# Performance work log

Measured on AMD Instinct MI355X. Metric: run time of the kernel, lower is better.

## Reference

```python
import jax, jax.numpy as jnp
import numpy as np

B, T, I, H, O = 32, 2048, 512, 512, 256


def setup_inputs() -> dict:
    key = jax.random.key(0)
    ks = jax.random.split(key, 11)
    s_in = 1.0 / np.sqrt(I)  # torch Linear default init bound
    s_h = 1.0 / np.sqrt(H)

    def lin(k, shape, s):
        return jax.random.uniform(k, shape, jnp.float32, -s, s)

    return {
        "x": jax.random.normal(ks[0], (B, T, I), jnp.float32),
        "W_i": lin(ks[1], (H, I), s_in), "b_i": lin(ks[2], (H,), s_in),
        "W_f": lin(ks[3], (H, I), s_in), "b_f": lin(ks[4], (H,), s_in),
        "W_g": lin(ks[5], (H, I), s_in), "b_g": lin(ks[6], (H,), s_in),
        "W_o": lin(ks[7], (H, I), s_in), "b_o": lin(ks[8], (H,), s_in),
        "W_fc": lin(ks[9], (O, H), s_h), "b_fc": lin(ks[10], (O,), s_h),
    }


def reference(x, W_i, b_i, W_f, b_f, W_g, b_g, W_o, b_o, W_fc, b_fc):
    # NOTE: this module's gates depend on x only (not h), so all four gate
    # projections can be precomputed as one pass of GEMMs over [B,T,I].
    gi = jax.nn.sigmoid(jnp.einsum("bti,hi->bth", x, W_i) + b_i)
    gf = jax.nn.sigmoid(jnp.einsum("bti,hi->bth", x, W_f) + b_f)
    gg = jnp.tanh(jnp.einsum("bti,hi->bth", x, W_g) + b_g)
    go = jax.nn.sigmoid(jnp.einsum("bti,hi->bth", x, W_o) + b_o)

    # Sequential elementwise recurrence over time (time-major for scan).
    def step(carry, gates_t):
        _, c = carry
        i, f, g, o = gates_t
        c = f * c + i * g
        h = o * jnp.tanh(c)
        return (h, c), None

    init = (jnp.zeros((B, H), x.dtype), jnp.zeros((B, H), x.dtype))
    gates_tm = (gi.swapaxes(0, 1), gf.swapaxes(0, 1),
                gg.swapaxes(0, 1), go.swapaxes(0, 1))  # each [T,B,H]
    (h, _), _ = jax.lax.scan(step, init, gates_tm)

    return h @ W_fc.T + b_fc  # [B, O]
```

## Files before the change

kernel.cpp:

```cpp
#include <hip/hip_runtime.h>
#include <stdint.h>

#define DI 512
#define DH 512
#define DOUT 256
#define NB 32
#define NT 2048
#define MTOT (NB*NT)
#define NCHUNK 16
#define CLEN 128
#define BM 128
#define BN 64
#define BK 32

typedef unsigned short u16;
typedef __attribute__((ext_vector_type(8))) short bf16x8;
typedef __attribute__((ext_vector_type(4))) short s16x4;
typedef __attribute__((ext_vector_type(4))) float f32x4;

__device__ __forceinline__ u16 f2bf(float f) {
    union { float f; unsigned int u; } c; c.f = f;
    unsigned int u = c.u;
    u += 0x7fffu + ((u >> 16) & 1u);
    return (u16)(u >> 16);
}
__device__ __forceinline__ float bf2f(u16 h) {
    union { unsigned int u; float f; } c; c.u = ((unsigned int)h) << 16;
    return c.f;
}
__device__ __forceinline__ float sigm(float x) { return 1.0f / (1.0f + __expf(-x)); }
__device__ __forceinline__ float tanh_(float x) { return 1.0f - 2.0f / (__expf(2.0f * x) + 1.0f); }

__global__ void cvt_w3(const float* __restrict__ w0, const float* __restrict__ w1,
                       const float* __restrict__ w2, u16* __restrict__ out) {
    const int per = DH * DI / 4;
    int gid = blockIdx.x * blockDim.x + threadIdx.x;
    int wsel = gid / per;
    int i = gid - wsel * per;
    const float* src = (wsel == 0) ? w0 : (wsel == 1) ? w1 : w2;
    float4 v = reinterpret_cast<const float4*>(src)[i];
    ushort4 o;
    o.x = f2bf(v.x); o.y = f2bf(v.y); o.z = f2bf(v.z); o.w = f2bf(v.w);
    reinterpret_cast<ushort4*>(out + (size_t)wsel * DH * DI)[i] = o;
}

__global__ __launch_bounds__(256, 2)
void gate_gemm_scan(const float* __restrict__ X, const u16* __restrict__ W,
                    const float* __restrict__ b_i, const float* __restrict__ b_f,
                    const float* __restrict__ b_g,
                    float* __restrict__ Ach, float* __restrict__ Vch) {
    __shared__ __align__(16) union {
        struct { u16 sA[2][BM * BK]; u16 sB[2][3 * BN * BK]; } st;
        struct { u16 Ft[BN][132]; u16 Pt[BN][132]; float pa[256]; float pv[256]; } sc;
    } u;

    const int bid0 = blockIdx.x;
    const int swz = (bid0 & 7) * 512 + (bid0 >> 3);
    const int mtile = swz >> 3;
    const int ntile = swz & 7;
    const int m0 = mtile * BM;
    const int n0 = ntile * BN;

    const int tid = threadIdx.x;
    const int lane = tid & 63;
    const int ws = __builtin_amdgcn_readfirstlane(tid >> 6);
    const int wr = ws >> 1;
    const int wc = ws & 1;

    const int srow = lane >> 2;
    const int slot = lane & 3;
    const int fr = lane & 15;
    const int khalf = lane >> 4;

    const int rlA = ws * 32 + srow;
    const int swzslot = slot ^ ((rlA >> 1) & 3);
    const float* pXA = X + (size_t)(m0 + rlA) * DI + swzslot * 8;

    const int idx0 = ws * 3;
    const int g0 = idx0 >> 2, cc0 = idx0 & 3;
    const int rlB0 = cc0 * 16 + srow;
    const u16* gaB0 = W + (size_t)g0 * DH * DI + (size_t)(n0 + rlB0) * DI
                    + ((slot ^ ((rlB0 >> 1) & 3)) * 8);
    int dB[3];
    dB[0] = 0;
#pragma unroll
    for (int q = 1; q < 3; ++q) {
        const int idxq = idx0 + q;
        const int gq = idxq >> 2, ccq = idxq & 3;
        dB[q] = __builtin_amdgcn_readfirstlane((gq - g0) * (DH * DI) + (ccq - cc0) * 16 * DI);
    }

    const int rA = wr * 64 + fr;
    const int offA0 = rA * BK + ((khalf ^ ((rA >> 1) & 3)) * 8);
    const int rB = wc * 32 + fr;
    const int offB0 = rB * BK + ((khalf ^ ((rB >> 1) & 3)) * 8);

    float4 fa[2][2][2];

#define LOAD_A(P, KT) do {                                                          \
    _Pragma("unroll")                                                               \
    for (int s = 0; s < 2; ++s) {                                                   \
        fa[(P)][s][0] = *reinterpret_cast<const float4*>(pXA + (size_t)s * 16 * DI + (KT) * 32);     \
        fa[(P)][s][1] = *reinterpret_cast<const float4*>(pXA + (size_t)s * 16 * DI + (KT) * 32 + 4); \
    }                                                                               \
} while (0)

#define CVT_STAGE(P, CB) do {                                                       \
    _Pragma("unroll")                                                               \
    for (int s = 0; s < 2; ++s) {                                                   \
        unsigned int pk0, pk1, pk2, pk3;                                            \
        asm("v_cvt_pk_bf16_f32 %0, %1, %2" : "=v"(pk0) : "v"(fa[(P)][s][0].x), "v"(fa[(P)][s][0].y)); \
        asm("v_cvt_pk_bf16_f32 %0, %1, %2" : "=v"(pk1) : "v"(fa[(P)][s][0].z), "v"(fa[(P)][s][0].w)); \
        asm("v_cvt_pk_bf16_f32 %0, %1, %2" : "=v"(pk2) : "v"(fa[(P)][s][1].x), "v"(fa[(P)][s][1].y)); \
        asm("v_cvt_pk_bf16_f32 %0, %1, %2" : "=v"(pk3) : "v"(fa[(P)][s][1].z), "v"(fa[(P)][s][1].w)); \
        uint4 wv; wv.x = pk0; wv.y = pk1; wv.z = pk2; wv.w = pk3;                   \
        *reinterpret_cast<uint4*>(u.st.sA[(CB)] + ((ws * 2 + s) * 512 + lane * 8)) = wv; \
    }                                                                               \
} while (0)

#define STAGE_B(CB, KT) do {                                                        \
    u16* sBb = u.st.sB[(CB)];                                                       \
    _Pragma("unroll")                                                               \
    for (int q = 0; q < 3; ++q) {                                                   \
        const int idxq = ws * 3 + q;                                                \
        __builtin_amdgcn_global_load_lds(                                           \
            (const __attribute__((address_space(1))) unsigned int*)(gaB0 + dB[q] + (KT) * BK), \
            (__attribute__((address_space(3))) unsigned int*)(sBb + (idxq >> 2) * (BN * BK) + (idxq & 3) * 512), \
            16, 0, 0);                                                              \
    }                                                                               \
} while (0)

    f32x4 acc[3][4][2] = {};

    LOAD_A(0, 0);
    LOAD_A(1, 1);
    CVT_STAGE(0, 0);
    STAGE_B(0, 0);
    asm volatile("s_waitcnt vmcnt(0)" ::: "memory");
    asm volatile("s_waitcnt lgkmcnt(0)" ::: "memory");
    __builtin_amdgcn_sched_barrier(0);
    __builtin_amdgcn_s_barrier();

#define KSTEP(KT) do {                                                              \
    constexpr int cur_ = (KT) & 1;                                                  \
    constexpr int nxt_ = cur_ ^ 1;                                                  \
    if ((KT) < 15) {                                                                \
        CVT_STAGE(nxt_, nxt_);       \
        STAGE_B(nxt_, (KT) + 1);                                                    \
    }                                                                               \
    if ((KT) < 14) LOAD_A(cur_, (KT) + 2);                                          \
    if ((KT) == 15) asm volatile("s_waitcnt vmcnt(0)" ::: "memory");                \
    __builtin_amdgcn_sched_barrier(0);                                              \
    __builtin_amdgcn_s_barrier();                                                   \
    {                                                                               \
        const u16* sAb = u.st.sA[cur_];                                             \
        const u16* sBb = u.st.sB[cur_];                                             \
        bf16x8 af[4];                                                               \
        _Pragma("unroll")                                                           \
        for (int m = 0; m < 4; m++)                                                 \
            af[m] = *reinterpret_cast<const bf16x8*>(sAb + offA0 + m * 16 * BK);    \
        __builtin_amdgcn_s_setprio(1);                                              \
        _Pragma("unroll")                                                           \
        for (int g = 0; g < 3; g++) {                                               \
            const u16* sbg = sBb + g * (BN * BK);                                   \
            bf16x8 b0 = *reinterpret_cast<const bf16x8*>(sbg + offB0);              \
            bf16x8 b1 = *reinterpret_cast<const bf16x8*>(sbg + offB0 + 16 * BK);    \
            _Pragma("unroll")                                                       \
            for (int m = 0; m < 4; m++) {                                           \
                acc[g][m][0] = __builtin_amdgcn_mfma_f32_16x16x32_bf16(af[m], b0, acc[g][m][0], 0, 0, 0); \
                acc[g][m][1] = __builtin_amdgcn_mfma_f32_16x16x32_bf16(af[m], b1, acc[g][m][1], 0, 0, 0); \
            }                                                                       \
        }                                                                           \
        __builtin_amdgcn_s_setprio(0);                                              \
    }                                                                               \
    if ((KT) < 15) {                                                                \
        asm volatile("s_waitcnt lgkmcnt(0)" ::: "memory");                          \
        __builtin_amdgcn_sched_barrier(0);                                          \
        __builtin_amdgcn_s_barrier();                                               \
    }                                                                               \
} while (0)

    KSTEP(0);  KSTEP(1);  KSTEP(2);  KSTEP(3);
    KSTEP(4);  KSTEP(5);  KSTEP(6);  KSTEP(7);
    KSTEP(8);  KSTEP(9);  KSTEP(10); KSTEP(11);
    KSTEP(12); KSTEP(13); KSTEP(14); KSTEP(15);
#undef KSTEP
#undef STAGE_B
#undef CVT_STAGE
#undef LOAD_A

    __syncthreads();

    const int rbase = (lane >> 4) * 4;
#pragma unroll
    for (int n = 0; n < 2; n++) {
        const int cl = wc * 32 + n * 16 + fr;
        const int hg = n0 + cl;
        const float bi_ = b_i[hg];
        const float bfv = b_f[hg];
        const float bg_ = b_g[hg];
#pragma unroll
        for (int m = 0; m < 4; m++) {
            const int rr0 = wr * 64 + m * 16 + rbase;
            s16x4 fpk, ppk;
#pragma unroll
            for (int jj = 0; jj < 4; jj++) {
                const float fi = sigm(acc[0][m][n][jj] + bi_);
                const float ff = sigm(acc[1][m][n][jj] + bfv);
                const float fg = tanh_(acc[2][m][n][jj] + bg_);
                fpk[jj] = (short)f2bf(ff);
                ppk[jj] = (short)f2bf(fi * fg);
            }
            *reinterpret_cast<s16x4*>(&u.sc.Ft[cl][rr0]) = fpk;
            *reinterpret_cast<s16x4*>(&u.sc.Pt[cl][rr0]) = ppk;
        }
    }
    __syncthreads();

    {
        const int h = tid & 63;
        const int q = tid >> 6;
        const int t0 = q * 32;
        float a = 1.0f, v = 0.0f;
#pragma unroll
        for (int kk = 0; kk < 8; kk++) {
            s16x4 fv = *reinterpret_cast<const s16x4*>(&u.sc.Ft[h][t0 + kk * 4]);
            s16x4 pv4 = *reinterpret_cast<const s16x4*>(&u.sc.Pt[h][t0 + kk * 4]);
#pragma unroll
            for (int e = 0; e < 4; e++) {
                const float f = bf2f((u16)fv[e]);
                const float p = bf2f((u16)pv4[e]);
                v = f * v + p;
                a *= f;
            }
        }
        u.sc.pa[tid] = a;
        u.sc.pv[tid] = v;
    }
    __syncthreads();

    if (tid < 64) {
        float Aacc = u.sc.pa[tid];
        float Vacc = u.sc.pv[tid];
#pragma unroll
        for (int q = 1; q < 4; q++) {
            const float aq = u.sc.pa[q * 64 + tid];
            const float vq = u.sc.pv[q * 64 + tid];
            Vacc = aq * Vacc + vq;
            Aacc *= aq;
        }
        const size_t o = (size_t)mtile * DH + n0 + tid;
        Ach[o] = Aacc;
        Vch[o] = Vacc;
    }
}

__global__ __launch_bounds__(512)
void finalize_fc(const float* __restrict__ Ach, const float* __restrict__ Vch,
                 const float* __restrict__ x, const float* __restrict__ Wo,
                 const float* __restrict__ bo, const float* __restrict__ Wfc,
                 const float* __restrict__ bfc, float* __restrict__ out) {
    __shared__ float xrow[DI];
    __shared__ float hrow[DH];
    const int b = blockIdx.x;
    const int tid = threadIdx.x;

    xrow[tid] = x[((size_t)b * NT + (NT - 1)) * DI + tid];
    float c = 0.0f;
#pragma unroll
    for (int jj = 0; jj < NCHUNK; jj++) {
        const size_t o = ((size_t)(b * NCHUNK + jj)) * DH + tid;
        c = Ach[o] * c + Vch[o];
    }
    __syncthreads();

    {
        const float4* xr = reinterpret_cast<const float4*>(xrow);
        const float4* wrow = reinterpret_cast<const float4*>(Wo + (size_t)tid * DI);
        float dot = 0.0f;
#pragma unroll 4
        for (int k = 0; k < DI / 4; k++) {
            float4 xv = xr[k];
            float4 wv = wrow[k];
            dot += xv.x * wv.x + xv.y * wv.y + xv.z * wv.z + xv.w * wv.w;
        }
        const float og = sigm(dot + bo[tid]);
        hrow[tid] = og * tanh_(c);
    }
    __syncthreads();

    if (tid < DOUT) {
        const float4* hr = reinterpret_cast<const float4*>(hrow);
        const float4* wrow = reinterpret_cast<const float4*>(Wfc + (size_t)tid * DH);
        float acc = 0.0f;
#pragma unroll 4
        for (int k = 0; k < DH / 4; k++) {
            float4 hv = hr[k];
            float4 wv = wrow[k];
            acc += hv.x * wv.x + hv.y * wv.y + hv.z * wv.z + hv.w * wv.w;
        }
        out[b * DOUT + tid] = acc + bfc[tid];
    }
}

extern "C" void kernel_launch(void* const* d_in, const int* in_sizes, int n_in,
                              void* d_out, int out_size, void* d_ws, size_t ws_size,
                              hipStream_t stream) {
    const float* x    = (const float*)d_in[0];
    const float* W_i  = (const float*)d_in[1];
    const float* b_i  = (const float*)d_in[2];
    const float* W_f  = (const float*)d_in[3];
    const float* b_f  = (const float*)d_in[4];
    const float* W_g  = (const float*)d_in[5];
    const float* b_g  = (const float*)d_in[6];
    const float* W_o  = (const float*)d_in[7];
    const float* b_o  = (const float*)d_in[8];
    const float* W_fc = (const float*)d_in[9];
    const float* b_fc = (const float*)d_in[10];
    float* out = (float*)d_out;

    char* ws = (char*)d_ws;
    u16* wbf    = (u16*)ws;
    float* Ach  = (float*)(ws + 1572864);
    float* Vch  = (float*)(ws + 2621440);

    cvt_w3<<<768, 256, 0, stream>>>(W_i, W_f, W_g, wbf);

    gate_gemm_scan<<<4096, 256, 0, stream>>>(x, wbf, b_i, b_f, b_g, Ach, Vch);

    finalize_fc<<<32, 512, 0, stream>>>(Ach, Vch, x, W_o, b_o, W_fc, b_fc, out);
}
```

Before: 201.6 us.

## Pre-convert x to bf16 and stream GEMM tiles via direct global-to-LDS loads

Adds a conversion kernel that writes x and the three gate weights to bf16 in the workspace. The gate GEMM then loads both operands with global_load_lds straight into shared memory, removing the in-kernel fp32-to-bf16 conversion and register staging, and raises the occupancy hint to 3 blocks. This costs an extra full read and write pass over the large x tensor, and the new path needs a large workspace; otherwise it falls back to the old fused kernel.

Result: no change. 199.4 us (-1.1%).

```diff
diff --git a/kernel.cpp b/kernel.cpp
--- a/kernel.cpp
+++ b/kernel.cpp
@@ -31,6 +31,232 @@
 __device__ __forceinline__ float sigm(float x) { return 1.0f / (1.0f + __expf(-x)); }
 __device__ __forceinline__ float tanh_(float x) { return 1.0f - 2.0f / (__expf(2.0f * x) + 1.0f); }
 
+__global__ __launch_bounds__(256)
+void cvt_all(const float* __restrict__ X, const float* __restrict__ w0,
+             const float* __restrict__ w1, const float* __restrict__ w2,
+             u16* __restrict__ xbf, u16* __restrict__ wbf) {
+    const int NX4 = MTOT * DI / 4;
+    const int NW4 = DH * DI / 4;
+    const int total = NX4 + 3 * NW4;
+    const int stride = gridDim.x * blockDim.x;
+    for (int i = blockIdx.x * blockDim.x + threadIdx.x; i < total; i += stride) {
+        const float4* s4; ushort4* d4; int j;
+        if (i < NX4) {
+            s4 = reinterpret_cast<const float4*>(X);
+            d4 = reinterpret_cast<ushort4*>(xbf);
+            j = i;
+        } else {
+            const int k = i - NX4;
+            const int w = k >> 16;
+            j = k & 65535;
+            s4 = reinterpret_cast<const float4*>(w == 0 ? w0 : w == 1 ? w1 : w2);
+            d4 = reinterpret_cast<ushort4*>(wbf + (size_t)w * DH * DI);
+        }
+        float4 v = s4[j];
+        unsigned int lo, hi;
+        asm("v_cvt_pk_bf16_f32 %0, %1, %2" : "=v"(lo) : "v"(v.x), "v"(v.y));
+        asm("v_cvt_pk_bf16_f32 %0, %1, %2" : "=v"(hi) : "v"(v.z), "v"(v.w));
+        ushort4 o;
+        o.x = (u16)(lo & 0xffffu); o.y = (u16)(lo >> 16);
+        o.z = (u16)(hi & 0xffffu); o.w = (u16)(hi >> 16);
+        d4[j] = o;
+    }
+}
+
+__global__ __launch_bounds__(256, 3)
+void gate_gemm_scan(const u16* __restrict__ Xbf, const u16* __restrict__ W,
+                    const float* __restrict__ b_i, const float* __restrict__ b_f,
+                    const float* __restrict__ b_g,
+                    float* __restrict__ Ach, float* __restrict__ Vch) {
+    __shared__ __align__(16) union {
+        struct { u16 sA[2][BM * BK]; u16 sB[2][3 * BN * BK]; } st;
+        struct { u16 Ft[BN][132]; u16 Pt[BN][132]; float pa[256]; float pv[256]; } sc;
+    } u;
+
+    const int bid0 = blockIdx.x;
+    const int swz = (bid0 & 7) * 512 + (bid0 >> 3);
+    const int mtile = swz >> 3;
+    const int ntile = swz & 7;
+    const int m0 = mtile * BM;
+    const int n0 = ntile * BN;
+
+    const int tid = threadIdx.x;
+    const int lane = tid & 63;
+    const int ws = __builtin_amdgcn_readfirstlane(tid >> 6);
+    const int wr = ws >> 1;
+    const int wc = ws & 1;
+
+    const int srow = lane >> 2;
+    const int slot = lane & 3;
+    const int fr = lane & 15;
+    const int khalf = lane >> 4;
+
+    const int rlA = ws * 32 + srow;
+    const int swzslot = slot ^ ((rlA >> 1) & 3);
+    const u16* pA0 = Xbf + (size_t)(m0 + rlA) * DI + swzslot * 8;
+    const u16* pA1 = pA0 + (size_t)16 * DI;
+
+    const int idx0 = ws * 3;
+    const int g0 = idx0 >> 2, cc0 = idx0 & 3;
+    const int rlB0 = cc0 * 16 + srow;
+    const u16* gaB0 = W + (size_t)g0 * DH * DI + (size_t)(n0 + rlB0) * DI
+                    + ((slot ^ ((rlB0 >> 1) & 3)) * 8);
+    int dB[3];
+    dB[0] = 0;
+#pragma unroll
+    for (int q = 1; q < 3; ++q) {
+        const int idxq = idx0 + q;
+        const int gq = idxq >> 2, ccq = idxq & 3;
+        dB[q] = __builtin_amdgcn_readfirstlane((gq - g0) * (DH * DI) + (ccq - cc0) * 16 * DI);
+    }
+
+    const int rA = wr * 64 + fr;
+    const int offA0 = rA * BK + ((khalf ^ ((rA >> 1) & 3)) * 8);
+    const int rB = wc * 32 + fr;
+    const int offB0 = rB * BK + ((khalf ^ ((rB >> 1) & 3)) * 8);
+
+#define STAGE_A(CB, KT) do {                                                        \
+    u16* sAb = u.st.sA[(CB)];                                                       \
+    __builtin_amdgcn_global_load_lds(                                               \
+        (const __attribute__((address_space(1))) unsigned int*)(pA0 + (KT) * BK),   \
+        (__attribute__((address_space(3))) unsigned int*)(sAb + (ws * 2 + 0) * 512),\
+        16, 0, 0);                                                                  \
+    __builtin_amdgcn_global_load_lds(                                               \
+        (const __attribute__((address_space(1))) unsigned int*)(pA1 + (KT) * BK),   \
+        (__attribute__((address_space(3))) unsigned int*)(sAb + (ws * 2 + 1) * 512),\
+        16, 0, 0);                                                                  \
+} while (0)
+
+#define STAGE_B(CB, KT) do {                                                        \
+    u16* sBb = u.st.sB[(CB)];                                                       \
+    _Pragma("unroll")                                                               \
+    for (int q = 0; q < 3; ++q) {                                                   \
+        const int idxq = ws * 3 + q;                                                \
+        __builtin_amdgcn_global_load_lds(                                           \
+            (const __attribute__((address_space(1))) unsigned int*)(gaB0 + dB[q] + (KT) * BK), \
+            (__attribute__((address_space(3))) unsigned int*)(sBb + (idxq >> 2) * (BN * BK) + (idxq & 3) * 512), \
+            16, 0, 0);                                                              \
+    }                                                                               \
+} while (0)
+
+    f32x4 acc[3][4][2] = {};
+
+    STAGE_A(0, 0);
+    STAGE_B(0, 0);
+
+#define KSTEP(KT) do {                                                              \
+    constexpr int cur_ = (KT) & 1;                                                  \
+    constexpr int nxt_ = cur_ ^ 1;                                                  \
+    if ((KT) < 15) {                                                                \
+        STAGE_A(nxt_, (KT) + 1);                                                    \
+        STAGE_B(nxt_, (KT) + 1);                                                    \
+        asm volatile("s_waitcnt vmcnt(5)" ::: "memory");                            \
+    } else {                                                                        \
+        asm volatile("s_waitcnt vmcnt(0)" ::: "memory");                            \
+    }                                                                               \
+    __builtin_amdgcn_sched_barrier(0);                                              \
+    __builtin_amdgcn_s_barrier();                                                   \
+    {                                                                               \
+        const u16* sAb = u.st.sA[cur_];                                             \
+        const u16* sBb = u.st.sB[cur_];                                             \
+        bf16x8 af[4];                                                               \
+        _Pragma("unroll")                                                           \
+        for (int m = 0; m < 4; m++)                                                 \
+            af[m] = *reinterpret_cast<const bf16x8*>(sAb + offA0 + m * 16 * BK);    \
+        __builtin_amdgcn_s_setprio(1);                                              \
+        _Pragma("unroll")                                                           \
+        for (int g = 0; g < 3; g++) {                                               \
+            const u16* sbg = sBb + g * (BN * BK);                                   \
+            bf16x8 b0 = *reinterpret_cast<const bf16x8*>(sbg + offB0);              \
+            bf16x8 b1 = *reinterpret_cast<const bf16x8*>(sbg + offB0 + 16 * BK);    \
+            _Pragma("unroll")                                                       \
+            for (int m = 0; m < 4; m++) {                                           \
+                acc[g][m][0] = __builtin_amdgcn_mfma_f32_16x16x32_bf16(af[m], b0, acc[g][m][0], 0, 0, 0); \
+                acc[g][m][1] = __builtin_amdgcn_mfma_f32_16x16x32_bf16(af[m], b1, acc[g][m][1], 0, 0, 0); \
+            }                                                                       \
+        }                                                                           \
+        __builtin_amdgcn_s_setprio(0);                                              \
+    }                                                                               \
+    if ((KT) < 15) {                                                                \
+        __builtin_amdgcn_sched_barrier(0);                                          \
+        __builtin_amdgcn_s_barrier();                                               \
+    }                                                                               \
+} while (0)
+
+    KSTEP(0);  KSTEP(1);  KSTEP(2);  KSTEP(3);
+    KSTEP(4);  KSTEP(5);  KSTEP(6);  KSTEP(7);
+    KSTEP(8);  KSTEP(9);  KSTEP(10); KSTEP(11);
+    KSTEP(12); KSTEP(13); KSTEP(14); KSTEP(15);
+#undef KSTEP
+#undef STAGE_B
+#undef STAGE_A
+
+    __syncthreads();
+
+    const int rbase = (lane >> 4) * 4;
+#pragma unroll
+    for (int n = 0; n < 2; n++) {
+        const int cl = wc * 32 + n * 16 + fr;
+        const int hg = n0 + cl;
+        const float bi_ = b_i[hg];
+        const float bfv = b_f[hg];
+        const float bg_ = b_g[hg];
+#pragma unroll
+        for (int m = 0; m < 4; m++) {
+            const int rr0 = wr * 64 + m * 16 + rbase;
+            s16x4 fpk, ppk;
+#pragma unroll
+            for (int jj = 0; jj < 4; jj++) {
+                const float fi = sigm(acc[0][m][n][jj] + bi_);
+                const float ff = sigm(acc[1][m][n][jj] + bfv);
+                const float fg = tanh_(acc[2][m][n][jj] + bg_);
+                fpk[jj] = (short)f2bf(ff);
+                ppk[jj] = (short)f2bf(fi * fg);
+            }
+            *reinterpret_cast<s16x4*>(&u.sc.Ft[cl][rr0]) = fpk;
+            *reinterpret_cast<s16x4*>(&u.sc.Pt[cl][rr0]) = ppk;
+        }
+    }
+    __syncthreads();
+
+    {
+        const int h = tid & 63;
+        const int q = tid >> 6;
+        const int t0 = q * 32;
+        float a = 1.0f, v = 0.0f;
+#pragma unroll
+        for (int kk = 0; kk < 8; kk++) {
+            s16x4 fv = *reinterpret_cast<const s16x4*>(&u.sc.Ft[h][t0 + kk * 4]);
+            s16x4 pv4 = *reinterpret_cast<const s16x4*>(&u.sc.Pt[h][t0 + kk * 4]);
+#pragma unroll
+            for (int e = 0; e < 4; e++) {
+                const float f = bf2f((u16)fv[e]);
+                const float p = bf2f((u16)pv4[e]);
+                v = f * v + p;
+                a *= f;
+            }
+        }
+        u.sc.pa[tid] = a;
+        u.sc.pv[tid] = v;
+    }
+    __syncthreads();
+
+    if (tid < 64) {
+        float Aacc = u.sc.pa[tid];
+        float Vacc = u.sc.pv[tid];
+#pragma unroll
+        for (int q = 1; q < 4; q++) {
+            const float aq = u.sc.pa[q * 64 + tid];
+            const float vq = u.sc.pv[q * 64 + tid];
+            Vacc = aq * Vacc + vq;
+            Aacc *= aq;
+        }
+        const size_t o = (size_t)mtile * DH + n0 + tid;
+        Ach[o] = Aacc;
+        Vch[o] = Vacc;
+    }
+}
+
 __global__ void cvt_w3(const float* __restrict__ w0, const float* __restrict__ w1,
                        const float* __restrict__ w2, u16* __restrict__ out) {
     const int per = DH * DI / 4;
@@ -45,10 +271,10 @@
 }
 
 __global__ __launch_bounds__(256, 2)
-void gate_gemm_scan(const float* __restrict__ X, const u16* __restrict__ W,
-                    const float* __restrict__ b_i, const float* __restrict__ b_f,
-                    const float* __restrict__ b_g,
-                    float* __restrict__ Ach, float* __restrict__ Vch) {
+void gate_gemm_scan_fused(const float* __restrict__ X, const u16* __restrict__ W,
+                          const float* __restrict__ b_i, const float* __restrict__ b_f,
+                          const float* __restrict__ b_g,
+                          float* __restrict__ Ach, float* __restrict__ Vch) {
     __shared__ __align__(16) union {
         struct { u16 sA[2][BM * BK]; u16 sB[2][3 * BN * BK]; } st;
         struct { u16 Ft[BN][132]; u16 Pt[BN][132]; float pa[256]; float pv[256]; } sc;
@@ -145,7 +371,7 @@
     constexpr int cur_ = (KT) & 1;                                                  \
     constexpr int nxt_ = cur_ ^ 1;                                                  \
     if ((KT) < 15) {                                                                \
-        CVT_STAGE(nxt_, nxt_);       \
+        CVT_STAGE(nxt_, nxt_);                                                      \
         STAGE_B(nxt_, (KT) + 1);                                                    \
     }                                                                               \
     if ((KT) < 14) LOAD_A(cur_, (KT) + 2);                                          \
@@ -320,13 +546,27 @@
     float* out = (float*)d_out;
 
     char* ws = (char*)d_ws;
-    u16* wbf    = (u16*)ws;
-    float* Ach  = (float*)(ws + 1572864);
-    float* Vch  = (float*)(ws + 2621440);
-
-    cvt_w3<<<768, 256, 0, stream>>>(W_i, W_f, W_g, wbf);
-
-    gate_gemm_scan<<<4096, 256, 0, stream>>>(x, wbf, b_i, b_f, b_g, Ach, Vch);
-
-    finalize_fc<<<32, 512, 0, stream>>>(Ach, Vch, x, W_o, b_o, W_fc, b_fc, out);
-}
+    const size_t XBF_BYTES = (size_t)MTOT * DI * 2;
+    const size_t WBF_BYTES = (size_t)3 * DH * DI * 2;
+    const size_t AV_BYTES  = (size_t)MTOT / CLEN * DH * 4;
+    const size_t NEED = XBF_BYTES + WBF_BYTES + 2 * AV_BYTES;
+
+    if (ws_size >= NEED) {
+        u16* xbf   = (u16*)ws;
+        u16* wbf   = (u16*)(ws + XBF_BYTES);
+        float* Ach = (float*)(ws + XBF_BYTES + WBF_BYTES);
+        float* Vch = (float*)(ws + XBF_BYTES + WBF_BYTES + AV_BYTES);
+
+        cvt_all<<<4096, 256, 0, stream>>>(x, W_i, W_f, W_g, xbf, wbf);
+        gate_gemm_scan<<<4096, 256, 0, stream>>>(xbf, wbf, b_i, b_f, b_g, Ach, Vch);
+        finalize_fc<<<32, 512, 0, stream>>>(Ach, Vch, x, W_o, b_o, W_fc, b_fc, out);
+    } else {
+        u16* wbf    = (u16*)ws;
+        float* Ach  = (float*)(ws + 1572864);
+        float* Vch  = (float*)(ws + 2621440);
+
+        cvt_w3<<<768, 256, 0, stream>>>(W_i, W_f, W_g, wbf);
+        gate_gemm_scan_fused<<<4096, 256, 0, stream>>>(x, wbf, b_i, b_f, b_g, Ach, Vch);
+        finalize_fc<<<32, 512, 0, stream>>>(Ach, Vch, x, W_o, b_o, W_fc, b_fc, out);
+    }
+}
```

## Stage fp32 X tiles directly into LDS and convert to bf16 at fragment load

Applied to the files above, without the earlier changes.

The A operand (fp32 activations) is now copied straight from global memory into LDS with global_load_lds and an XOR-swizzled layout, instead of passing through registers for bf16 conversion before the LDS write. The bf16 packing moves to after the LDS fragment read in each k-step, and the wait/barrier scheme changes to a partial vmcnt wait. This is meant to cut register pressure and VALU/LDS-store work in the producer path, at the cost of doubling the LDS footprint for A and adding conversion work in the MFMA loop. Separately, the finalize kernel issues all chunk loads before running the serial combine, so those loads can overlap.

After: 211.8 us. 5.1% more time.

```diff
diff --git a/kernel.cpp b/kernel.cpp
--- a/kernel.cpp
+++ b/kernel.cpp
@@ -50,7 +50,7 @@
                     const float* __restrict__ b_g,
                     float* __restrict__ Ach, float* __restrict__ Vch) {
     __shared__ __align__(16) union {
-        struct { u16 sA[2][BM * BK]; u16 sB[2][3 * BN * BK]; } st;
+        struct { float sA[2][BM * BK]; u16 sB[2][3 * BN * BK]; } st;
         struct { u16 Ft[BN][132]; u16 Pt[BN][132]; float pa[256]; float pv[256]; } sc;
     } u;
 
@@ -72,9 +72,9 @@
     const int fr = lane & 15;
     const int khalf = lane >> 4;
 
-    const int rlA = ws * 32 + srow;
-    const int swzslot = slot ^ ((rlA >> 1) & 3);
-    const float* pXA = X + (size_t)(m0 + rlA) * DI + swzslot * 8;
+    const int lr = lane >> 3;
+    const int s8 = lane & 7;
+    const float* pAf = X + (size_t)(m0 + ws * 32 + lr) * DI + ((s8 ^ lr) * 4);
 
     const int idx0 = ws * 3;
     const int g0 = idx0 >> 2, cc0 = idx0 & 3;
@@ -90,31 +90,20 @@
         dB[q] = __builtin_amdgcn_readfirstlane((gq - g0) * (DH * DI) + (ccq - cc0) * 16 * DI);
     }
 
-    const int rA = wr * 64 + fr;
-    const int offA0 = rA * BK + ((khalf ^ ((rA >> 1) & 3)) * 8);
+    const int sl0 = (khalf * 2) ^ (fr & 7);
+    const int offAf0 = (wr * 64 + fr) * BK + sl0 * 4;
+    const int offAf1 = (wr * 64 + fr) * BK + (sl0 ^ 1) * 4;
     const int rB = wc * 32 + fr;
     const int offB0 = rB * BK + ((khalf ^ ((rB >> 1) & 3)) * 8);
 
-    float4 fa[2][2][2];
-
-#define LOAD_A(P, KT) do {                                                          \
+#define STAGE_A(CB, KT) do {                                                        \
+    float* sAb = u.st.sA[(CB)];                                                     \
     _Pragma("unroll")                                                               \
-    for (int s = 0; s < 2; ++s) {                                                   \
-        fa[(P)][s][0] = *reinterpret_cast<const float4*>(pXA + (size_t)s * 16 * DI + (KT) * 32);     \
-        fa[(P)][s][1] = *reinterpret_cast<const float4*>(pXA + (size_t)s * 16 * DI + (KT) * 32 + 4); \
-    }                                                                               \
-} while (0)
-
-#define CVT_STAGE(P, CB) do {                                                       \
-    _Pragma("unroll")                                                               \
-    for (int s = 0; s < 2; ++s) {                                                   \
-        unsigned int pk0, pk1, pk2, pk3;                                            \
-        asm("v_cvt_pk_bf16_f32 %0, %1, %2" : "=v"(pk0) : "v"(fa[(P)][s][0].x), "v"(fa[(P)][s][0].y)); \
-        asm("v_cvt_pk_bf16_f32 %0, %1, %2" : "=v"(pk1) : "v"(fa[(P)][s][0].z), "v"(fa[(P)][s][0].w)); \
-        asm("v_cvt_pk_bf16_f32 %0, %1, %2" : "=v"(pk2) : "v"(fa[(P)][s][1].x), "v"(fa[(P)][s][1].y)); \
-        asm("v_cvt_pk_bf16_f32 %0, %1, %2" : "=v"(pk3) : "v"(fa[(P)][s][1].z), "v"(fa[(P)][s][1].w)); \
-        uint4 wv; wv.x = pk0; wv.y = pk1; wv.z = pk2; wv.w = pk3;                   \
-        *reinterpret_cast<uint4*>(u.st.sA[(CB)] + ((ws * 2 + s) * 512 + lane * 8)) = wv; \
+    for (int j = 0; j < 4; ++j) {                                                   \
+        __builtin_amdgcn_global_load_lds(                                           \
+            (const __attribute__((address_space(1))) unsigned int*)(pAf + (size_t)j * 8 * DI + (KT) * BK), \
+            (__attribute__((address_space(3))) unsigned int*)(sAb + (ws * 32 + j * 8) * BK), \
+            16, 0, 0);                                                              \
     }                                                                               \
 } while (0)
 
@@ -132,33 +121,38 @@
 
     f32x4 acc[3][4][2] = {};
 
-    LOAD_A(0, 0);
-    LOAD_A(1, 1);
-    CVT_STAGE(0, 0);
+    STAGE_A(0, 0);
     STAGE_B(0, 0);
-    asm volatile("s_waitcnt vmcnt(0)" ::: "memory");
-    asm volatile("s_waitcnt lgkmcnt(0)" ::: "memory");
-    __builtin_amdgcn_sched_barrier(0);
-    __builtin_amdgcn_s_barrier();
 
 #define KSTEP(KT) do {                                                              \
     constexpr int cur_ = (KT) & 1;                                                  \
     constexpr int nxt_ = cur_ ^ 1;                                                  \
     if ((KT) < 15) {                                                                \
-        CVT_STAGE(nxt_, nxt_);       \
+        STAGE_A(nxt_, (KT) + 1);                                                    \
         STAGE_B(nxt_, (KT) + 1);                                                    \
-    }                                                                               \
-    if ((KT) < 14) LOAD_A(cur_, (KT) + 2);                                          \
-    if ((KT) == 15) asm volatile("s_waitcnt vmcnt(0)" ::: "memory");                \
+        asm volatile("s_waitcnt vmcnt(7)" ::: "memory");                            \
+    } else {                                                                        \
+        asm volatile("s_waitcnt vmcnt(0)" ::: "memory");                            \
+    }                                                                               \
     __builtin_amdgcn_sched_barrier(0);                                              \
     __builtin_amdgcn_s_barrier();                                                   \
     {                                                                               \
-        const u16* sAb = u.st.sA[cur_];                                             \
+        const float* sAf = u.st.sA[cur_];                                           \
         const u16* sBb = u.st.sB[cur_];                                             \
         bf16x8 af[4];                                                               \
         _Pragma("unroll")                                                           \
-        for (int m = 0; m < 4; m++)                                                 \
-            af[m] = *reinterpret_cast<const bf16x8*>(sAb + offA0 + m * 16 * BK);    \
+        for (int m = 0; m < 4; m++) {                                               \
+            f32x4 a0 = *reinterpret_cast<const f32x4*>(sAf + offAf0 + m * 16 * BK); \
+            f32x4 a1 = *reinterpret_cast<const f32x4*>(sAf + offAf1 + m * 16 * BK); \
+            unsigned int q0, q1, q2, q3;                                            \
+            asm("v_cvt_pk_bf16_f32 %0, %1, %2" : "=v"(q0) : "v"(a0[0]), "v"(a0[1])); \
+            asm("v_cvt_pk_bf16_f32 %0, %1, %2" : "=v"(q1) : "v"(a0[2]), "v"(a0[3])); \
+            asm("v_cvt_pk_bf16_f32 %0, %1, %2" : "=v"(q2) : "v"(a1[0]), "v"(a1[1])); \
+            asm("v_cvt_pk_bf16_f32 %0, %1, %2" : "=v"(q3) : "v"(a1[2]), "v"(a1[3])); \
+            union { bf16x8 v; unsigned int w[4]; } cc;                              \
+            cc.w[0] = q0; cc.w[1] = q1; cc.w[2] = q2; cc.w[3] = q3;                 \
+            af[m] = cc.v;                                                           \
+        }                                                                           \
         __builtin_amdgcn_s_setprio(1);                                              \
         _Pragma("unroll")                                                           \
         for (int g = 0; g < 3; g++) {                                               \
@@ -174,7 +168,6 @@
         __builtin_amdgcn_s_setprio(0);                                              \
     }                                                                               \
     if ((KT) < 15) {                                                                \
-        asm volatile("s_waitcnt lgkmcnt(0)" ::: "memory");                          \
         __builtin_amdgcn_sched_barrier(0);                                          \
         __builtin_amdgcn_s_barrier();                                               \
     }                                                                               \
@@ -186,8 +179,7 @@
     KSTEP(12); KSTEP(13); KSTEP(14); KSTEP(15);
 #undef KSTEP
 #undef STAGE_B
-#undef CVT_STAGE
-#undef LOAD_A
+#undef STAGE_A
 
     __syncthreads();
 
@@ -266,12 +258,16 @@
     const int tid = threadIdx.x;
 
     xrow[tid] = x[((size_t)b * NT + (NT - 1)) * DI + tid];
-    float c = 0.0f;
+    float av[NCHUNK], vv[NCHUNK];
 #pragma unroll
     for (int jj = 0; jj < NCHUNK; jj++) {
         const size_t o = ((size_t)(b * NCHUNK + jj)) * DH + tid;
-        c = Ach[o] * c + Vch[o];
-    }
+        av[jj] = Ach[o];
+        vv[jj] = Vch[o];
+    }
+    float c = 0.0f;
+#pragma unroll
+    for (int jj = 0; jj < NCHUNK; jj++) c = av[jj] * c + vv[jj];
     __syncthreads();
 
     {
```

## Pre-convert X to bf16 and stage A tiles via direct global-to-LDS loads

Applied to the files above, without the earlier changes.

Adds a separate conversion pass that writes the whole input X as bf16 to workspace. The gate GEMM then stages its A tiles with global_load_lds, the same way as the weights, instead of loading fp32 into registers and converting in-loop. This frees registers, so occupancy is raised to 3 blocks per CU. The cost is an extra full pass over X: a 128MB read plus a 64MB write. The finalize step is also split into two kernels (h computation and FC) spread over more blocks with LDS tiling.

New measurement: 174.4 us. 1.16x faster.

```diff
diff --git a/kernel.cpp b/kernel.cpp
--- a/kernel.cpp
+++ b/kernel.cpp
@@ -31,21 +31,43 @@
 __device__ __forceinline__ float sigm(float x) { return 1.0f / (1.0f + __expf(-x)); }
 __device__ __forceinline__ float tanh_(float x) { return 1.0f - 2.0f / (__expf(2.0f * x) + 1.0f); }
 
-__global__ void cvt_w3(const float* __restrict__ w0, const float* __restrict__ w1,
-                       const float* __restrict__ w2, u16* __restrict__ out) {
-    const int per = DH * DI / 4;
-    int gid = blockIdx.x * blockDim.x + threadIdx.x;
-    int wsel = gid / per;
-    int i = gid - wsel * per;
-    const float* src = (wsel == 0) ? w0 : (wsel == 1) ? w1 : w2;
-    float4 v = reinterpret_cast<const float4*>(src)[i];
-    ushort4 o;
-    o.x = f2bf(v.x); o.y = f2bf(v.y); o.z = f2bf(v.z); o.w = f2bf(v.w);
-    reinterpret_cast<ushort4*>(out + (size_t)wsel * DH * DI)[i] = o;
-}
-
-__global__ __launch_bounds__(256, 2)
-void gate_gemm_scan(const float* __restrict__ X, const u16* __restrict__ W,
+__global__ __launch_bounds__(256)
+void cvt_all2(const float* __restrict__ X, const float* __restrict__ w0,
+              const float* __restrict__ w1, const float* __restrict__ w2,
+              u16* __restrict__ xbf, u16* __restrict__ wbf) {
+    const int bid = blockIdx.x;
+    const int tid = threadIdx.x;
+    if (bid < 4096) {
+        const int idx = bid * 256 + tid;
+        const float4* s4 = reinterpret_cast<const float4*>(X);
+        uint4* d4 = reinterpret_cast<uint4*>(xbf);
+#pragma unroll
+        for (int it = 0; it < 4; ++it) {
+            const int j = it * 1048576 + idx;
+            float4 v0 = s4[2 * j];
+            float4 v1 = s4[2 * j + 1];
+            unsigned int p0, p1, p2, p3;
+            asm("v_cvt_pk_bf16_f32 %0, %1, %2" : "=v"(p0) : "v"(v0.x), "v"(v0.y));
+            asm("v_cvt_pk_bf16_f32 %0, %1, %2" : "=v"(p1) : "v"(v0.z), "v"(v0.w));
+            asm("v_cvt_pk_bf16_f32 %0, %1, %2" : "=v"(p2) : "v"(v1.x), "v"(v1.y));
+            asm("v_cvt_pk_bf16_f32 %0, %1, %2" : "=v"(p3) : "v"(v1.z), "v"(v1.w));
+            uint4 o; o.x = p0; o.y = p1; o.z = p2; o.w = p3;
+            d4[j] = o;
+        }
+    } else {
+        const int gid = (bid - 4096) * 256 + tid;
+        const int wsel = gid >> 16;
+        const int i = gid & 65535;
+        const float* src = (wsel == 0) ? w0 : (wsel == 1) ? w1 : w2;
+        float4 v = reinterpret_cast<const float4*>(src)[i];
+        ushort4 o;
+        o.x = f2bf(v.x); o.y = f2bf(v.y); o.z = f2bf(v.z); o.w = f2bf(v.w);
+        reinterpret_cast<ushort4*>(wbf + (size_t)wsel * DH * DI)[i] = o;
+    }
+}
+
+__global__ __launch_bounds__(256, 3)
+void gate_gemm_scan(const u16* __restrict__ Xbf, const u16* __restrict__ W,
                     const float* __restrict__ b_i, const float* __restrict__ b_f,
                     const float* __restrict__ b_g,
                     float* __restrict__ Ach, float* __restrict__ Vch) {
@@ -74,7 +96,8 @@
 
     const int rlA = ws * 32 + srow;
     const int swzslot = slot ^ ((rlA >> 1) & 3);
-    const float* pXA = X + (size_t)(m0 + rlA) * DI + swzslot * 8;
+    const u16* pA0 = Xbf + (size_t)(m0 + rlA) * DI + swzslot * 8;
+    const u16* pA1 = pA0 + (size_t)16 * DI;
 
     const int idx0 = ws * 3;
     const int g0 = idx0 >> 2, cc0 = idx0 & 3;
@@ -95,27 +118,16 @@
     const int rB = wc * 32 + fr;
     const int offB0 = rB * BK + ((khalf ^ ((rB >> 1) & 3)) * 8);
 
-    float4 fa[2][2][2];
-
-#define LOAD_A(P, KT) do {                                                          \
-    _Pragma("unroll")                                                               \
-    for (int s = 0; s < 2; ++s) {                                                   \
-        fa[(P)][s][0] = *reinterpret_cast<const float4*>(pXA + (size_t)s * 16 * DI + (KT) * 32);     \
-        fa[(P)][s][1] = *reinterpret_cast<const float4*>(pXA + (size_t)s * 16 * DI + (KT) * 32 + 4); \
-    }                                                                               \
-} while (0)
-
-#define CVT_STAGE(P, CB) do {                                                       \
-    _Pragma("unroll")                                                               \
-    for (int s = 0; s < 2; ++s) {                                                   \
-        unsigned int pk0, pk1, pk2, pk3;                                            \
-        asm("v_cvt_pk_bf16_f32 %0, %1, %2" : "=v"(pk0) : "v"(fa[(P)][s][0].x), "v"(fa[(P)][s][0].y)); \
-        asm("v_cvt_pk_bf16_f32 %0, %1, %2" : "=v"(pk1) : "v"(fa[(P)][s][0].z), "v"(fa[(P)][s][0].w)); \
-        asm("v_cvt_pk_bf16_f32 %0, %1, %2" : "=v"(pk2) : "v"(fa[(P)][s][1].x), "v"(fa[(P)][s][1].y)); \
-        asm("v_cvt_pk_bf16_f32 %0, %1, %2" : "=v"(pk3) : "v"(fa[(P)][s][1].z), "v"(fa[(P)][s][1].w)); \
-        uint4 wv; wv.x = pk0; wv.y = pk1; wv.z = pk2; wv.w = pk3;                   \
-        *reinterpret_cast<uint4*>(u.st.sA[(CB)] + ((ws * 2 + s) * 512 + lane * 8)) = wv; \
-    }                                                                               \
+#define STAGE_A(CB, KT) do {                                                        \
+    u16* sAb = u.st.sA[(CB)];                                                       \
+    __builtin_amdgcn_global_load_lds(                                               \
+        (const __attribute__((address_space(1))) unsigned int*)(pA0 + (KT) * BK),   \
+        (__attribute__((address_space(3))) unsigned int*)(sAb + (ws * 2 + 0) * 512),\
+        16, 0, 0);                                                                  \
+    __builtin_amdgcn_global_load_lds(                                               \
+        (const __attribute__((address_space(1))) unsigned int*)(pA1 + (KT) * BK),   \
+        (__attribute__((address_space(3))) unsigned int*)(sAb + (ws * 2 + 1) * 512),\
+        16, 0, 0);                                                                  \
 } while (0)
 
 #define STAGE_B(CB, KT) do {                                                        \
@@ -132,24 +144,19 @@
 
     f32x4 acc[3][4][2] = {};
 
-    LOAD_A(0, 0);
-    LOAD_A(1, 1);
-    CVT_STAGE(0, 0);
+    STAGE_A(0, 0);
     STAGE_B(0, 0);
-    asm volatile("s_waitcnt vmcnt(0)" ::: "memory");
-    asm volatile("s_waitcnt lgkmcnt(0)" ::: "memory");
-    __builtin_amdgcn_sched_barrier(0);
-    __builtin_amdgcn_s_barrier();
 
 #define KSTEP(KT) do {                                                              \
     constexpr int cur_ = (KT) & 1;                                                  \
     constexpr int nxt_ = cur_ ^ 1;                                                  \
     if ((KT) < 15) {                                                                \
-        CVT_STAGE(nxt_, nxt_);       \
+        STAGE_A(nxt_, (KT) + 1);                                                    \
         STAGE_B(nxt_, (KT) + 1);                                                    \
+        asm volatile("s_waitcnt vmcnt(5)" ::: "memory");                            \
+    } else {                                                                        \
+        asm volatile("s_waitcnt vmcnt(0)" ::: "memory");                            \
     }                                                                               \
-    if ((KT) < 14) LOAD_A(cur_, (KT) + 2);                                          \
-    if ((KT) == 15) asm volatile("s_waitcnt vmcnt(0)" ::: "memory");                \
     __builtin_amdgcn_sched_barrier(0);                                              \
     __builtin_amdgcn_s_barrier();                                                   \
     {                                                                               \
@@ -174,7 +181,6 @@
         __builtin_amdgcn_s_setprio(0);                                              \
     }                                                                               \
     if ((KT) < 15) {                                                                \
-        asm volatile("s_waitcnt lgkmcnt(0)" ::: "memory");                          \
         __builtin_amdgcn_sched_barrier(0);                                          \
         __builtin_amdgcn_s_barrier();                                               \
     }                                                                               \
@@ -186,8 +192,7 @@
     KSTEP(12); KSTEP(13); KSTEP(14); KSTEP(15);
 #undef KSTEP
 #undef STAGE_B
-#undef CVT_STAGE
-#undef LOAD_A
+#undef STAGE_A
 
     __syncthreads();
 
@@ -255,52 +260,100 @@
     }
 }
 
-__global__ __launch_bounds__(512)
-void finalize_fc(const float* __restrict__ Ach, const float* __restrict__ Vch,
-                 const float* __restrict__ x, const float* __restrict__ Wo,
-                 const float* __restrict__ bo, const float* __restrict__ Wfc,
-                 const float* __restrict__ bfc, float* __restrict__ out) {
-    __shared__ float xrow[DI];
-    __shared__ float hrow[DH];
-    const int b = blockIdx.x;
+__global__ __launch_bounds__(256)
+void finalize_h(const float* __restrict__ Ach, const float* __restrict__ Vch,
+                const float* __restrict__ x, const float* __restrict__ Wo,
+                const float* __restrict__ bo, float* __restrict__ hval) {
+    __shared__ float woT[8][512];
+    __shared__ float xl[32][129];
     const int tid = threadIdx.x;
-
-    xrow[tid] = x[((size_t)b * NT + (NT - 1)) * DI + tid];
+    const int h0 = blockIdx.x * 8;
+    const int hloc = tid >> 5;
+    const int b = tid & 31;
+    const int h = h0 + hloc;
+
+    {
+        const int r = tid >> 5, q = tid & 31;
+#pragma unroll
+        for (int m = 0; m < 4; m++) {
+            float4 v = reinterpret_cast<const float4*>(Wo + (size_t)(h0 + r) * DI)[q + 32 * m];
+            *reinterpret_cast<float4*>(&woT[r][4 * (q + 32 * m)]) = v;
+        }
+    }
+
     float c = 0.0f;
 #pragma unroll
     for (int jj = 0; jj < NCHUNK; jj++) {
-        const size_t o = ((size_t)(b * NCHUNK + jj)) * DH + tid;
+        const size_t o = ((size_t)(b * NCHUNK + jj)) * DH + h;
         c = Ach[o] * c + Vch[o];
     }
-    __syncthreads();
+
+    float dot = 0.0f;
+    const float* xlast = x + ((size_t)b * NT + (NT - 1)) * DI;
+    for (int kc = 0; kc < 4; kc++) {
+        __syncthreads();
+        {
+            const int r = tid >> 3, s = tid & 7;
+            const float* xr = x + ((size_t)r * NT + (NT - 1)) * DI + kc * 128;
+#pragma unroll
+            for (int m = 0; m < 4; m++) {
+                float4 v = reinterpret_cast<const float4*>(xr)[s + 8 * m];
+                const int cbase = 4 * (s + 8 * m);
+                xl[r][cbase + 0] = v.x; xl[r][cbase + 1] = v.y;
+                xl[r][cbase + 2] = v.z; xl[r][cbase + 3] = v.w;
+            }
+        }
+        __syncthreads();
+#pragma unroll 8
+        for (int k = 0; k < 128; k++)
+            dot += woT[hloc][kc * 128 + k] * xl[b][k];
+        (void)xlast;
+    }
+
+    const float og = sigm(dot + bo[h]);
+    hval[(size_t)b * DH + h] = og * tanh_(c);
+}
+
+__global__ __launch_bounds__(256)
+void finalize_fc2(const float* __restrict__ hval, const float* __restrict__ Wfc,
+                  const float* __restrict__ bfc, float* __restrict__ out) {
+    __shared__ float wf[8][512];
+    __shared__ float hl[32][129];
+    const int tid = threadIdx.x;
+    const int o0 = blockIdx.x * 8;
+    const int oloc = tid >> 5;
+    const int b = tid & 31;
 
     {
-        const float4* xr = reinterpret_cast<const float4*>(xrow);
-        const float4* wrow = reinterpret_cast<const float4*>(Wo + (size_t)tid * DI);
-        float dot = 0.0f;
-#pragma unroll 4
-        for (int k = 0; k < DI / 4; k++) {
-            float4 xv = xr[k];
-            float4 wv = wrow[k];
-            dot += xv.x * wv.x + xv.y * wv.y + xv.z * wv.z + xv.w * wv.w;
-        }
-        const float og = sigm(dot + bo[tid]);
-        hrow[tid] = og * tanh_(c);
-    }
-    __syncthreads();
-
-    if (tid < DOUT) {
-        const float4* hr = reinterpret_cast<const float4*>(hrow);
-        const float4* wrow = reinterpret_cast<const float4*>(Wfc + (size_t)tid * DH);
-        float acc = 0.0f;
-#pragma unroll 4
-        for (int k = 0; k < DH / 4; k++) {
-            float4 hv = hr[k];
-            float4 wv = wrow[k];
-            acc += hv.x * wv.x + hv.y * wv.y + hv.z * wv.z + hv.w * wv.w;
-        }
-        out[b * DOUT + tid] = acc + bfc[tid];
-    }
+        const int r = tid >> 5, q = tid & 31;
+#pragma unroll
+        for (int m = 0; m < 4; m++) {
+            float4 v = reinterpret_cast<const float4*>(Wfc + (size_t)(o0 + r) * DH)[q + 32 * m];
+            *reinterpret_cast<float4*>(&wf[r][4 * (q + 32 * m)]) = v;
+        }
+    }
+
+    float acc = 0.0f;
+    for (int kc = 0; kc < 4; kc++) {
+        __syncthreads();
+        {
+            const int r = tid >> 3, s = tid & 7;
+            const float* hr = hval + (size_t)r * DH + kc * 128;
+#pragma unroll
+            for (int m = 0; m < 4; m++) {
+                float4 v = reinterpret_cast<const float4*>(hr)[s + 8 * m];
+                const int cbase = 4 * (s + 8 * m);
+                hl[r][cbase + 0] = v.x; hl[r][cbase + 1] = v.y;
+                hl[r][cbase + 2] = v.z; hl[r][cbase + 3] = v.w;
+            }
+        }
+        __syncthreads();
+#pragma unroll 8
+        for (int k = 0; k < 128; k++)
+            acc += wf[oloc][kc * 128 + k] * hl[b][k];
+    }
+
+    out[b * DOUT + (o0 + oloc)] = acc + bfc[o0 + oloc];
 }
 
 extern "C" void kernel_launch(void* const* d_in, const int* in_sizes, int n_in,
@@ -320,13 +373,21 @@
     float* out = (float*)d_out;
 
     char* ws = (char*)d_ws;
-    u16* wbf    = (u16*)ws;
-    float* Ach  = (float*)(ws + 1572864);
-    float* Vch  = (float*)(ws + 2621440);
-
-    cvt_w3<<<768, 256, 0, stream>>>(W_i, W_f, W_g, wbf);
-
-    gate_gemm_scan<<<4096, 256, 0, stream>>>(x, wbf, b_i, b_f, b_g, Ach, Vch);
-
-    finalize_fc<<<32, 512, 0, stream>>>(Ach, Vch, x, W_o, b_o, W_fc, b_fc, out);
-}
+    const size_t XBF_BYTES = (size_t)MTOT * DI * 2;
+    const size_t WBF_BYTES = (size_t)3 * DH * DI * 2;
+    const size_t AV_BYTES  = (size_t)MTOT / CLEN * DH * 4;
+
+    u16* xbf   = (u16*)ws;
+    u16* wbf   = (u16*)(ws + XBF_BYTES);
+    float* Ach = (float*)(ws + XBF_BYTES + WBF_BYTES);
+    float* Vch = (float*)(ws + XBF_BYTES + WBF_BYTES + AV_BYTES);
+    float* hval = (float*)(ws + XBF_BYTES);
+
+    cvt_all2<<<4864, 256, 0, stream>>>(x, W_i, W_f, W_g, xbf, wbf);
+
+    gate_gemm_scan<<<4096, 256, 0, stream>>>(xbf, wbf, b_i, b_f, b_g, Ach, Vch);
+
+    finalize_h<<<64, 256, 0, stream>>>(Ach, Vch, x, W_o, b_o, hval);
+
+    finalize_fc2<<<32, 256, 0, stream>>>(hval, W_fc, b_fc, out);
+}
```
